# Optimization experiments

Hardware: AMD Instinct MI355X
Metric: run time of the kernel (lower is better)

## Reference

```python
import jax, jax.numpy as jnp
import numpy as np

N = 50000   # nodes
E = 800000  # edges
D = 64      # attrs_dim
H = 128     # 2*attrs_dim (GIN MLP hidden)
L = 3       # gnn_layers_num
G = 128     # graphs in batch


def setup_inputs() -> dict:
    key = jax.random.key(0)
    ks = jax.random.split(key, 9)
    s = 0.1
    attrs = jax.random.normal(ks[0], (N, D), dtype=jnp.float32)
    edge_index = jax.random.randint(ks[1], (2, E), 0, N, dtype=jnp.int64)
    batch = jnp.sort(jax.random.randint(ks[2], (N,), 0, G, dtype=jnp.int64))
    W1 = jax.random.normal(ks[3], (L, D, H), dtype=jnp.float32) * s
    b1 = jnp.zeros((L, H), jnp.float32)
    W2 = jax.random.normal(ks[4], (L, H, H), dtype=jnp.float32) * s
    b2 = jnp.zeros((L, H), jnp.float32)
    W3 = jax.random.normal(ks[5], (L, H, D), dtype=jnp.float32) * s
    b3 = jnp.zeros((L, D), jnp.float32)
    return {"attrs": attrs, "W1": W1, "b1": b1, "W2": W2, "b2": b2,
            "W3": W3, "b3": b3, "edge_index": edge_index, "batch": batch}


def reference(attrs, W1, b1, W2, b2, W3, b3, edge_index, batch):
    src, dst = edge_index[0], edge_index[1]
    x = attrs
    for l in range(L):  # small fixed layer count
        # GINConv with eps=0: MLP(x + sum_{j->i} x_j)
        agg = jax.ops.segment_sum(x[src], dst, num_segments=N)
        h = x + agg
        # MLP with tanh after each linear (per MLP.forward)
        h = jnp.tanh(h @ W1[l] + b1[l])
        h = jnp.tanh(h @ W2[l] + b2[l])
        h = jnp.tanh(h @ W3[l] + b3[l])
        # outer activation in GNN.forward
        x = jnp.tanh(h)
    # scatter_mean over graph ids
    sums = jax.ops.segment_sum(x, batch, num_segments=G)          # [G, D]
    counts = jax.ops.segment_sum(jnp.ones((N,), x.dtype), batch, num_segments=G)
    return sums / jnp.maximum(counts, 1.0)[:, None]
```

## Files before the change

kernel.cpp:

```cpp
#include <hip/hip_runtime.h>
#include <math.h>

#define N_NODES 50000
#define N_EDGES 800000
#define DIM 64
#define HID 128
#define LAYERS 3
#define NGRAPH 128

#define SCAN_TILE 1024
#define SCAN_NB ((N_NODES + SCAN_TILE - 1) / SCAN_TILE)

typedef __attribute__((ext_vector_type(8))) short short8v;
typedef __attribute__((ext_vector_type(4))) float f32x4;

__device__ __forceinline__ float bf2f(unsigned short u) {
    return __uint_as_float(((unsigned)u) << 16);
}
__device__ __forceinline__ unsigned short f2bf(float x) {
    unsigned u = __float_as_uint(x);
    unsigned r = (u + 0x7fff + ((u >> 16) & 1)) >> 16;
    return (unsigned short)r;
}
__device__ __forceinline__ float fast_tanh(float x) {
    float xc = fminf(fmaxf(x, -9.0f), 9.0f);
    float y = __expf(2.0f * xc);
    return 1.0f - 2.0f * __builtin_amdgcn_rcpf(y + 1.0f);
}

__global__ void count_kernel(const int* __restrict__ dst,
                             int* __restrict__ counts,
                             unsigned short* __restrict__ rank) {
    int e = (blockIdx.x * blockDim.x + threadIdx.x) * 2;
    if (e + 1 < N_EDGES) {
        int d0 = dst[e], d1 = dst[e + 1];
        int r0 = atomicAdd(&counts[d0], 1);
        int r1 = atomicAdd(&counts[d1], 1);
        rank[e]     = (unsigned short)r0;
        rank[e + 1] = (unsigned short)r1;
    } else if (e < N_EDGES) {
        rank[e] = (unsigned short)atomicAdd(&counts[dst[e]], 1);
    }
}

__global__ void scan_partial_kernel(const int* __restrict__ counts,
                                    int* __restrict__ bsum) {
    __shared__ int red[256];
    const int b = blockIdx.x, tid = threadIdx.x;
    const int base = b * SCAN_TILE + tid * 4;
    int s = 0;
    if (base + 3 < N_NODES) {
        int4 v = *reinterpret_cast<const int4*>(counts + base);
        s = v.x + v.y + v.z + v.w;
    } else {
        for (int i = 0; i < 4; ++i)
            if (base + i < N_NODES) s += counts[base + i];
    }
    red[tid] = s;
    __syncthreads();
    for (int off = 128; off > 0; off >>= 1) {
        if (tid < off) red[tid] += red[tid + off];
        __syncthreads();
    }
    if (tid == 0) bsum[b] = red[0];
}

__global__ void scan_mid_kernel(const int* __restrict__ bsum,
                                int* __restrict__ bpre,
                                int* __restrict__ offsets) {
    int tid = threadIdx.x;
    int orig = (tid < SCAN_NB) ? bsum[tid] : 0;
    int v = orig;
    for (int off = 1; off < 64; off <<= 1) {
        int u = __shfl_up(v, off);
        if (tid >= off) v += u;
    }
    if (tid < SCAN_NB) bpre[tid] = v - orig;
    if (tid == 0) offsets[N_NODES] = N_EDGES;
}

__global__ void scan_final_kernel(const int* __restrict__ counts,
                                  const int* __restrict__ bpre,
                                  int* __restrict__ offsets) {
    __shared__ int pre[256];
    const int b = blockIdx.x, tid = threadIdx.x;
    const int base = b * SCAN_TILE + tid * 4;
    int c[4];
    int s = 0;
#pragma unroll
    for (int i = 0; i < 4; ++i) {
        c[i] = (base + i < N_NODES) ? counts[base + i] : 0;
        s += c[i];
    }
    pre[tid] = s;
    __syncthreads();
    for (int off = 1; off < 256; off <<= 1) {
        int v = (tid >= off) ? pre[tid - off] : 0;
        __syncthreads();
        pre[tid] += v;
        __syncthreads();
    }
    int run = bpre[b] + pre[tid] - s;
#pragma unroll
    for (int i = 0; i < 4; ++i) {
        if (base + i < N_NODES) {
            offsets[base + i] = run;
            run += c[i];
        }
    }
}

__global__ void place_kernel(const int* __restrict__ src,
                             const int* __restrict__ dst,
                             const unsigned short* __restrict__ rank,
                             const int* __restrict__ offsets,
                             unsigned short* __restrict__ csr_src) {
    int e = blockIdx.x * blockDim.x + threadIdx.x;
    if (e >= N_EDGES) return;
    csr_src[offsets[dst[e]] + (int)rank[e]] = (unsigned short)src[e];
}

template<int K, int C>
__device__ __forceinline__ void repack_one(const float* __restrict__ W,
                                           unsigned short* __restrict__ P, int t) {
    constexpr int KT = K / 32, CT = C / 16;
    int lane = t & 63; int rest = t >> 6;
    int ct = rest % CT; rest /= CT;
    int kt = rest % KT; int l = rest / KT;
    int li = lane & 15, hi = lane >> 4;
    const float* Wl = W + (size_t)l * K * C;
    short8v o;
#pragma unroll
    for (int j = 0; j < 8; ++j)
        o[j] = (short)f2bf(Wl[(size_t)(kt * 32 + hi * 8 + j) * C + ct * 16 + li]);
    *reinterpret_cast<short8v*>(P + ((size_t)l * KT * CT * 64 + (size_t)(kt * CT + ct) * 64 + lane) * 8) = o;
}

__global__ void repack_all_kernel(const float* __restrict__ W1, const float* __restrict__ W2,
                                  const float* __restrict__ W3,
                                  unsigned short* __restrict__ P1, unsigned short* __restrict__ P2,
                                  unsigned short* __restrict__ P3) {
    int t = blockIdx.x * 256 + threadIdx.x;
    if (t < 3072)       repack_one<DIM, HID>(W1, P1, t);
    else if (t < 9216)  repack_one<HID, HID>(W2, P2, t - 3072);
    else                repack_one<HID, DIM>(W3, P3, t - 9216);
}

template<bool F32IN, bool LAST>
__global__ __launch_bounds__(256) void gnn_layer_kernel(
        const float* __restrict__ xf, const unsigned short* __restrict__ xb,
        const int* __restrict__ offsets, const unsigned short* __restrict__ csr_src,
        const unsigned short* __restrict__ pw1, const float* __restrict__ bias1,
        const unsigned short* __restrict__ pw2, const float* __restrict__ bias2,
        const unsigned short* __restrict__ pw3, const float* __restrict__ bias3,
        unsigned short* __restrict__ outx,
        const int* __restrict__ batch, float* __restrict__ psums) {
    __shared__ float aggA[16 * 68];
    __shared__ float aggB[16 * 68];
    __shared__ unsigned short tileA[16 * 128];
    __shared__ unsigned short tileB[16 * 128];
    __shared__ int soff[17];
    const int tid = threadIdx.x;
    const int wave = tid >> 6, lane = tid & 63;
    const int li = lane & 15, hi = lane >> 4;
    const int r0 = blockIdx.x * 16;
    char* tA = reinterpret_cast<char*>(tileA);
    char* tB = reinterpret_cast<char*>(tileB);

    if (tid < 17) soff[tid] = offsets[r0 + tid];
    __syncthreads();

    {
        const int g  = tid >> 3;
        const int nr = g >> 1;
        const int h  = g & 1;
        const int q  = tid & 7;
        const int n  = r0 + nr;
        float a[8];
        if (h == 0) {
            if (F32IN) {
                const float* xr = xf + (size_t)n * DIM + q * 8;
                float4 u = *reinterpret_cast<const float4*>(xr);
                float4 w = *reinterpret_cast<const float4*>(xr + 4);
                a[0]=u.x; a[1]=u.y; a[2]=u.z; a[3]=u.w;
                a[4]=w.x; a[5]=w.y; a[6]=w.z; a[7]=w.w;
            } else {
                short8v v = *reinterpret_cast<const short8v*>(xb + (size_t)n * DIM + q * 8);
#pragma unroll
                for (int j = 0; j < 8; ++j) a[j] = bf2f((unsigned short)v[j]);
            }
        } else {
#pragma unroll
            for (int j = 0; j < 8; ++j) a[j] = 0.f;
        }
        const int p0 = soff[nr], pe1 = soff[nr + 1];
        const int mid = p0 + ((pe1 - p0 + 1) >> 1);
        int p        = h ? mid : p0;
        const int pe = h ? pe1 : mid;
        for (; p + 4 <= pe; p += 4) {
            int s0 = csr_src[p + 0];
            int s1 = csr_src[p + 1];
            int s2 = csr_src[p + 2];
            int s3 = csr_src[p + 3];
            if (F32IN) {
                const float* x0 = xf + (size_t)s0 * DIM + q * 8;
                const float* x1 = xf + (size_t)s1 * DIM + q * 8;
                const float* x2 = xf + (size_t)s2 * DIM + q * 8;
                const float* x3 = xf + (size_t)s3 * DIM + q * 8;
                float4 u0 = *reinterpret_cast<const float4*>(x0);
                float4 w0 = *reinterpret_cast<const float4*>(x0 + 4);
                float4 u1 = *reinterpret_cast<const float4*>(x1);
                float4 w1 = *reinterpret_cast<const float4*>(x1 + 4);
                float4 u2 = *reinterpret_cast<const float4*>(x2);
                float4 w2 = *reinterpret_cast<const float4*>(x2 + 4);
                float4 u3 = *reinterpret_cast<const float4*>(x3);
                float4 w3 = *reinterpret_cast<const float4*>(x3 + 4);
                a[0] += u0.x + u1.x + u2.x + u3.x;
                a[1] += u0.y + u1.y + u2.y + u3.y;
                a[2] += u0.z + u1.z + u2.z + u3.z;
                a[3] += u0.w + u1.w + u2.w + u3.w;
                a[4] += w0.x + w1.x + w2.x + w3.x;
                a[5] += w0.y + w1.y + w2.y + w3.y;
                a[6] += w0.z + w1.z + w2.z + w3.z;
                a[7] += w0.w + w1.w + w2.w + w3.w;
            } else {
                short8v v0 = *reinterpret_cast<const short8v*>(xb + (size_t)s0 * DIM + q * 8);
                short8v v1 = *reinterpret_cast<const short8v*>(xb + (size_t)s1 * DIM + q * 8);
                short8v v2 = *reinterpret_cast<const short8v*>(xb + (size_t)s2 * DIM + q * 8);
                short8v v3 = *reinterpret_cast<const short8v*>(xb + (size_t)s3 * DIM + q * 8);
#pragma unroll
                for (int j = 0; j < 8; ++j)
                    a[j] += bf2f((unsigned short)v0[j]) + bf2f((unsigned short)v1[j])
                          + bf2f((unsigned short)v2[j]) + bf2f((unsigned short)v3[j]);
            }
        }
        for (; p < pe; ++p) {
            int s = csr_src[p];
            if (F32IN) {
                const float* xs = xf + (size_t)s * DIM + q * 8;
                float4 u = *reinterpret_cast<const float4*>(xs);
                float4 w = *reinterpret_cast<const float4*>(xs + 4);
                a[0] += u.x; a[1] += u.y; a[2] += u.z; a[3] += u.w;
                a[4] += w.x; a[5] += w.y; a[6] += w.z; a[7] += w.w;
            } else {
                short8v v = *reinterpret_cast<const short8v*>(xb + (size_t)s * DIM + q * 8);
#pragma unroll
                for (int j = 0; j < 8; ++j) a[j] += bf2f((unsigned short)v[j]);
            }
        }
        float* d = (h ? aggB : aggA) + nr * 68 + q * 8;
        *reinterpret_cast<f32x4*>(d)     = (f32x4){a[0], a[1], a[2], a[3]};
        *reinterpret_cast<f32x4*>(d + 4) = (f32x4){a[4], a[5], a[6], a[7]};
    }
    __syncthreads();

    short8v af[2];
#pragma unroll
    for (int kt = 0; kt < 2; ++kt) {
        const float* sA = &aggA[li * 68 + kt * 32 + hi * 8];
        const float* sB = &aggB[li * 68 + kt * 32 + hi * 8];
#pragma unroll
        for (int j = 0; j < 8; ++j) af[kt][j] = (short)f2bf(sA[j] + sB[j]);
    }

    f32x4 acc1[2];
#pragma unroll
    for (int c = 0; c < 2; ++c) acc1[c] = (f32x4){0.f, 0.f, 0.f, 0.f};
#pragma unroll
    for (int c = 0; c < 2; ++c) {
        const int ct = 2 * wave + c;
#pragma unroll
        for (int kt = 0; kt < 2; ++kt) {
            short8v bfr = *reinterpret_cast<const short8v*>(pw1 + ((size_t)(kt * 8 + ct) * 64 + lane) * 8);
            acc1[c] = __builtin_amdgcn_mfma_f32_16x16x32_bf16(af[kt], bfr, acc1[c], 0, 0, 0);
        }
    }
#pragma unroll
    for (int c = 0; c < 2; ++c) {
        const int ct = 2 * wave + c;
        float bv = bias1[ct * 16 + li];
#pragma unroll
        for (int j = 0; j < 4; ++j) {
            int row = hi * 4 + j;
            unsigned off = (unsigned)(row * 256 + (ct * 16 + li) * 2) ^ ((unsigned)(row & 7) << 4);
            *reinterpret_cast<unsigned short*>(tA + off) = f2bf(fast_tanh(acc1[c][j] + bv));
        }
    }
    __syncthreads();

    short8v af2[4];
#pragma unroll
    for (int kt = 0; kt < 4; ++kt) {
        unsigned off = (unsigned)(li * 256 + (kt * 32 + hi * 8) * 2) ^ ((unsigned)(li & 7) << 4);
        af2[kt] = *reinterpret_cast<const short8v*>(tA + off);
    }
    f32x4 acc2[2];
#pragma unroll
    for (int c = 0; c < 2; ++c) acc2[c] = (f32x4){0.f, 0.f, 0.f, 0.f};
#pragma unroll
    for (int c = 0; c < 2; ++c) {
        const int ct = 2 * wave + c;
#pragma unroll
        for (int kt = 0; kt < 4; ++kt) {
            short8v bfr = *reinterpret_cast<const short8v*>(pw2 + ((size_t)(kt * 8 + ct) * 64 + lane) * 8);
            acc2[c] = __builtin_amdgcn_mfma_f32_16x16x32_bf16(af2[kt], bfr, acc2[c], 0, 0, 0);
        }
    }
#pragma unroll
    for (int c = 0; c < 2; ++c) {
        const int ct = 2 * wave + c;
        float bv = bias2[ct * 16 + li];
#pragma unroll
        for (int j = 0; j < 4; ++j) {
            int row = hi * 4 + j;
            unsigned off = (unsigned)(row * 256 + (ct * 16 + li) * 2) ^ ((unsigned)(row & 7) << 4);
            *reinterpret_cast<unsigned short*>(tB + off) = f2bf(fast_tanh(acc2[c][j] + bv));
        }
    }
    __syncthreads();

    short8v af3[4];
#pragma unroll
    for (int kt = 0; kt < 4; ++kt) {
        unsigned off = (unsigned)(li * 256 + (kt * 32 + hi * 8) * 2) ^ ((unsigned)(li & 7) << 4);
        af3[kt] = *reinterpret_cast<const short8v*>(tB + off);
    }
    f32x4 acc3 = (f32x4){0.f, 0.f, 0.f, 0.f};
#pragma unroll
    for (int kt = 0; kt < 4; ++kt) {
        short8v bfr = *reinterpret_cast<const short8v*>(pw3 + ((size_t)(kt * 4 + wave) * 64 + lane) * 8);
        acc3 = __builtin_amdgcn_mfma_f32_16x16x32_bf16(af3[kt], bfr, acc3, 0, 0, 0);
    }
    {
        const int c = wave * 16 + li;
        float bv = bias3[c];
        if (LAST) {
            const int row0 = r0 + hi * 4;
            float v[4];
#pragma unroll
            for (int j = 0; j < 4; ++j) v[j] = fast_tanh(fast_tanh(acc3[j] + bv));
            int g = batch[row0];
            float acc = v[0];
#pragma unroll
            for (int j = 1; j < 4; ++j) {
                int gj = batch[row0 + j];
                if (gj == g) acc += v[j];
                else {
                    atomicAdd(&psums[g * DIM + c], acc);
                    g = gj; acc = v[j];
                }
            }
            atomicAdd(&psums[g * DIM + c], acc);
        } else {
#pragma unroll
            for (int j = 0; j < 4; ++j) {
                int row = r0 + hi * 4 + j;
                float vv = fast_tanh(fast_tanh(acc3[j] + bv));
                outx[(size_t)row * DIM + c] = f2bf(vv);
            }
        }
    }
}

__global__ void pool_final_kernel(const float* __restrict__ sums,
                                  const int* __restrict__ batch,
                                  float* __restrict__ out) {
    const int g = blockIdx.x;
    const int d = threadIdx.x;
    int lo = 0, hi = N_NODES;
    while (lo < hi) { int m = (lo + hi) >> 1; if (batch[m] < g) lo = m + 1; else hi = m; }
    int start = lo;
    hi = N_NODES;
    while (lo < hi) { int m = (lo + hi) >> 1; if (batch[m] < g + 1) lo = m + 1; else hi = m; }
    float cnt = (float)(lo - start);
    out[g * DIM + d] = sums[g * DIM + d] / fmaxf(cnt, 1.f);
}

extern "C" void kernel_launch(void* const* d_in, const int* in_sizes, int n_in,
                              void* d_out, int out_size, void* d_ws, size_t ws_size,
                              hipStream_t stream) {
    const float* attrs = (const float*)d_in[0];
    const float* W1    = (const float*)d_in[1];
    const float* b1    = (const float*)d_in[2];
    const float* W2    = (const float*)d_in[3];
    const float* b2    = (const float*)d_in[4];
    const float* W3    = (const float*)d_in[5];
    const float* b3    = (const float*)d_in[6];
    const int* edge_index = (const int*)d_in[7];
    const int* batch      = (const int*)d_in[8];
    float* out = (float*)d_out;

    unsigned short* buf0 = (unsigned short*)d_ws;
    unsigned short* buf1 = buf0 + (size_t)N_NODES * DIM;
    unsigned short* pW1  = buf1 + (size_t)N_NODES * DIM;
    unsigned short* pW2  = pW1 + 24576;
    unsigned short* pW3  = pW2 + 49152;
    float* psums  = (float*)(pW3 + 24576);
    int* offsets  = (int*)(psums + NGRAPH * DIM);
    unsigned short* csr16 = (unsigned short*)(offsets + N_NODES + 1);
    unsigned short* rank  = csr16 + N_EDGES;
    int* counts   = (int*)(rank + N_EDGES);
    int* bsum     = counts + N_NODES;
    int* bpre     = bsum + SCAN_NB;

    const int* src = edge_index;
    const int* dst = edge_index + N_EDGES;

    const int edge_blocks  = (N_EDGES + 255) / 256;
    const int count_blocks = (N_EDGES / 2 + 255) / 256;
    const int gnn_blocks   = N_NODES / 16;

    hipMemsetAsync(counts, 0, (size_t)N_NODES * sizeof(int), stream);
    hipMemsetAsync(psums, 0, (size_t)NGRAPH * DIM * sizeof(float), stream);
    count_kernel<<<count_blocks, 256, 0, stream>>>(dst, counts, rank);
    scan_partial_kernel<<<SCAN_NB, 256, 0, stream>>>(counts, bsum);
    scan_mid_kernel<<<1, 64, 0, stream>>>(bsum, bpre, offsets);
    scan_final_kernel<<<SCAN_NB, 256, 0, stream>>>(counts, bpre, offsets);
    place_kernel<<<edge_blocks, 256, 0, stream>>>(src, dst, rank, offsets, csr16);

    repack_all_kernel<<<48, 256, 0, stream>>>(W1, W2, W3, pW1, pW2, pW3);

    for (int l = 0; l < LAYERS; ++l) {
        const unsigned short* w1 = pW1 + (size_t)l * 2 * 8 * 64 * 8;
        const unsigned short* w2 = pW2 + (size_t)l * 4 * 8 * 64 * 8;
        const unsigned short* w3 = pW3 + (size_t)l * 4 * 4 * 64 * 8;
        const float* bb1 = b1 + (size_t)l * HID;
        const float* bb2 = b2 + (size_t)l * HID;
        const float* bb3 = b3 + (size_t)l * DIM;
        if (l == 0)
            gnn_layer_kernel<true, false><<<gnn_blocks, 256, 0, stream>>>(
                attrs, nullptr, offsets, csr16, w1, bb1, w2, bb2, w3, bb3,
                buf0, nullptr, nullptr);
        else if (l == 1)
            gnn_layer_kernel<false, false><<<gnn_blocks, 256, 0, stream>>>(
                nullptr, buf0, offsets, csr16, w1, bb1, w2, bb2, w3, bb3,
                buf1, nullptr, nullptr);
        else
            gnn_layer_kernel<false, true><<<gnn_blocks, 256, 0, stream>>>(
                nullptr, buf1, offsets, csr16, w1, bb1, w2, bb2, w3, bb3,
                nullptr, batch, psums);
    }

    pool_final_kernel<<<NGRAPH, DIM, 0, stream>>>(psums, batch, out);
}
```

Before: 183.4 us.

## Convert input to bf16, split aggregation 4-way with 512-thread blocks, fuse scan

Adds a pre-pass that converts the fp32 node attributes to bf16, so the first layer gathers half as many bytes per neighbour. The GNN layer kernel now runs 512 threads per 16-node tile, splits each node's edge list into four quarters instead of two, and gives each of 8 waves one MFMA column tile. The separate scan_mid kernel is removed: each scan_final block sums the preceding block totals serially. place_kernel now handles two edges per thread. The costs are an extra conversion kernel, bf16 rounding of the layer-0 input, and idle waves during the third matmul.

New measurement: 195.9 us. 6.8% more time.

```diff
diff --git a/kernel.cpp b/kernel.cpp
--- a/kernel.cpp
+++ b/kernel.cpp
@@ -26,6 +26,19 @@
     float xc = fminf(fmaxf(x, -9.0f), 9.0f);
     float y = __expf(2.0f * xc);
     return 1.0f - 2.0f * __builtin_amdgcn_rcpf(y + 1.0f);
+}
+
+__global__ void cvt_kernel(const float* __restrict__ a, unsigned short* __restrict__ b) {
+    int i = blockIdx.x * blockDim.x + threadIdx.x;
+    if (i >= N_NODES * DIM / 8) return;
+    const float4* p = reinterpret_cast<const float4*>(a + (size_t)i * 8);
+    float4 u = p[0], w = p[1];
+    short8v o;
+    o[0] = (short)f2bf(u.x); o[1] = (short)f2bf(u.y);
+    o[2] = (short)f2bf(u.z); o[3] = (short)f2bf(u.w);
+    o[4] = (short)f2bf(w.x); o[5] = (short)f2bf(w.y);
+    o[6] = (short)f2bf(w.z); o[7] = (short)f2bf(w.w);
+    *reinterpret_cast<short8v*>(b + (size_t)i * 8) = o;
 }
 
 __global__ void count_kernel(const int* __restrict__ dst,
@@ -65,25 +78,18 @@
     if (tid == 0) bsum[b] = red[0];
 }
 
-__global__ void scan_mid_kernel(const int* __restrict__ bsum,
-                                int* __restrict__ bpre,
-                                int* __restrict__ offsets) {
-    int tid = threadIdx.x;
-    int orig = (tid < SCAN_NB) ? bsum[tid] : 0;
-    int v = orig;
-    for (int off = 1; off < 64; off <<= 1) {
-        int u = __shfl_up(v, off);
-        if (tid >= off) v += u;
-    }
-    if (tid < SCAN_NB) bpre[tid] = v - orig;
-    if (tid == 0) offsets[N_NODES] = N_EDGES;
-}
-
 __global__ void scan_final_kernel(const int* __restrict__ counts,
-                                  const int* __restrict__ bpre,
+                                  const int* __restrict__ bsum,
                                   int* __restrict__ offsets) {
     __shared__ int pre[256];
+    __shared__ int bbase;
     const int b = blockIdx.x, tid = threadIdx.x;
+    if (tid == 0) {
+        int s = 0;
+        for (int i = 0; i < b; ++i) s += bsum[i];
+        bbase = s;
+        if (b == SCAN_NB - 1) offsets[N_NODES] = N_EDGES;
+    }
     const int base = b * SCAN_TILE + tid * 4;
     int c[4];
     int s = 0;
@@ -100,7 +106,7 @@
         pre[tid] += v;
         __syncthreads();
     }
-    int run = bpre[b] + pre[tid] - s;
+    int run = bbase + pre[tid] - s;
 #pragma unroll
     for (int i = 0; i < 4; ++i) {
         if (base + i < N_NODES) {
@@ -115,9 +121,15 @@
                              const unsigned short* __restrict__ rank,
                              const int* __restrict__ offsets,
                              unsigned short* __restrict__ csr_src) {
-    int e = blockIdx.x * blockDim.x + threadIdx.x;
-    if (e >= N_EDGES) return;
-    csr_src[offsets[dst[e]] + (int)rank[e]] = (unsigned short)src[e];
+    int e = (blockIdx.x * blockDim.x + threadIdx.x) * 2;
+    if (e + 1 < N_EDGES) {
+        int d0 = dst[e], d1 = dst[e + 1];
+        int o0 = offsets[d0], o1 = offsets[d1];
+        csr_src[o0 + (int)rank[e]]     = (unsigned short)src[e];
+        csr_src[o1 + (int)rank[e + 1]] = (unsigned short)src[e + 1];
+    } else if (e < N_EDGES) {
+        csr_src[offsets[dst[e]] + (int)rank[e]] = (unsigned short)src[e];
+    }
 }
 
 template<int K, int C>
@@ -146,17 +158,16 @@
     else                repack_one<HID, DIM>(W3, P3, t - 9216);
 }
 
-template<bool F32IN, bool LAST>
-__global__ __launch_bounds__(256) void gnn_layer_kernel(
-        const float* __restrict__ xf, const unsigned short* __restrict__ xb,
+template<bool LAST>
+__global__ __launch_bounds__(512) void gnn_layer_kernel(
+        const unsigned short* __restrict__ xb,
         const int* __restrict__ offsets, const unsigned short* __restrict__ csr_src,
         const unsigned short* __restrict__ pw1, const float* __restrict__ bias1,
         const unsigned short* __restrict__ pw2, const float* __restrict__ bias2,
         const unsigned short* __restrict__ pw3, const float* __restrict__ bias3,
         unsigned short* __restrict__ outx,
         const int* __restrict__ batch, float* __restrict__ psums) {
-    __shared__ float aggA[16 * 68];
-    __shared__ float aggB[16 * 68];
+    __shared__ float aggQ[4][16 * 68];
     __shared__ unsigned short tileA[16 * 128];
     __shared__ unsigned short tileB[16 * 128];
     __shared__ int soff[17];
@@ -172,118 +183,75 @@
 
     {
         const int g  = tid >> 3;
-        const int nr = g >> 1;
-        const int h  = g & 1;
+        const int nr = g >> 2;
+        const int h  = g & 3;
         const int q  = tid & 7;
         const int n  = r0 + nr;
         float a[8];
         if (h == 0) {
-            if (F32IN) {
-                const float* xr = xf + (size_t)n * DIM + q * 8;
-                float4 u = *reinterpret_cast<const float4*>(xr);
-                float4 w = *reinterpret_cast<const float4*>(xr + 4);
-                a[0]=u.x; a[1]=u.y; a[2]=u.z; a[3]=u.w;
-                a[4]=w.x; a[5]=w.y; a[6]=w.z; a[7]=w.w;
-            } else {
-                short8v v = *reinterpret_cast<const short8v*>(xb + (size_t)n * DIM + q * 8);
-#pragma unroll
-                for (int j = 0; j < 8; ++j) a[j] = bf2f((unsigned short)v[j]);
-            }
+            short8v v = *reinterpret_cast<const short8v*>(xb + (size_t)n * DIM + q * 8);
+#pragma unroll
+            for (int j = 0; j < 8; ++j) a[j] = bf2f((unsigned short)v[j]);
         } else {
 #pragma unroll
             for (int j = 0; j < 8; ++j) a[j] = 0.f;
         }
-        const int p0 = soff[nr], pe1 = soff[nr + 1];
-        const int mid = p0 + ((pe1 - p0 + 1) >> 1);
-        int p        = h ? mid : p0;
-        const int pe = h ? pe1 : mid;
+        const int p0 = soff[nr];
+        const int d  = soff[nr + 1] - p0;
+        int p        = p0 + ((d * h) >> 2);
+        const int pe = p0 + ((d * (h + 1)) >> 2);
         for (; p + 4 <= pe; p += 4) {
             int s0 = csr_src[p + 0];
             int s1 = csr_src[p + 1];
             int s2 = csr_src[p + 2];
             int s3 = csr_src[p + 3];
-            if (F32IN) {
-                const float* x0 = xf + (size_t)s0 * DIM + q * 8;
-                const float* x1 = xf + (size_t)s1 * DIM + q * 8;
-                const float* x2 = xf + (size_t)s2 * DIM + q * 8;
-                const float* x3 = xf + (size_t)s3 * DIM + q * 8;
-                float4 u0 = *reinterpret_cast<const float4*>(x0);
-                float4 w0 = *reinterpret_cast<const float4*>(x0 + 4);
-                float4 u1 = *reinterpret_cast<const float4*>(x1);
-                float4 w1 = *reinterpret_cast<const float4*>(x1 + 4);
-                float4 u2 = *reinterpret_cast<const float4*>(x2);
-                float4 w2 = *reinterpret_cast<const float4*>(x2 + 4);
-                float4 u3 = *reinterpret_cast<const float4*>(x3);
-                float4 w3 = *reinterpret_cast<const float4*>(x3 + 4);
-                a[0] += u0.x + u1.x + u2.x + u3.x;
-                a[1] += u0.y + u1.y + u2.y + u3.y;
-                a[2] += u0.z + u1.z + u2.z + u3.z;
-                a[3] += u0.w + u1.w + u2.w + u3.w;
-                a[4] += w0.x + w1.x + w2.x + w3.x;
-                a[5] += w0.y + w1.y + w2.y + w3.y;
-                a[6] += w0.z + w1.z + w2.z + w3.z;
-                a[7] += w0.w + w1.w + w2.w + w3.w;
-            } else {
-                short8v v0 = *reinterpret_cast<const short8v*>(xb + (size_t)s0 * DIM + q * 8);
-                short8v v1 = *reinterpret_cast<const short8v*>(xb + (size_t)s1 * DIM + q * 8);
-                short8v v2 = *reinterpret_cast<const short8v*>(xb + (size_t)s2 * DIM + q * 8);
-                short8v v3 = *reinterpret_cast<const short8v*>(xb + (size_t)s3 * DIM + q * 8);
-#pragma unroll
-                for (int j = 0; j < 8; ++j)
-                    a[j] += bf2f((unsigned short)v0[j]) + bf2f((unsigned short)v1[j])
-                          + bf2f((unsigned short)v2[j]) + bf2f((unsigned short)v3[j]);
-            }
+            short8v v0 = *reinterpret_cast<const short8v*>(xb + (size_t)s0 * DIM + q * 8);
+            short8v v1 = *reinterpret_cast<const short8v*>(xb + (size_t)s1 * DIM + q * 8);
+            short8v v2 = *reinterpret_cast<const short8v*>(xb + (size_t)s2 * DIM + q * 8);
+            short8v v3 = *reinterpret_cast<const short8v*>(xb + (size_t)s3 * DIM + q * 8);
+#pragma unroll
+            for (int j = 0; j < 8; ++j)
+                a[j] += bf2f((unsigned short)v0[j]) + bf2f((unsigned short)v1[j])
+                      + bf2f((unsigned short)v2[j]) + bf2f((unsigned short)v3[j]);
         }
         for (; p < pe; ++p) {
             int s = csr_src[p];
-            if (F32IN) {
-                const float* xs = xf + (size_t)s * DIM + q * 8;
-                float4 u = *reinterpret_cast<const float4*>(xs);
-                float4 w = *reinterpret_cast<const float4*>(xs + 4);
-                a[0] += u.x; a[1] += u.y; a[2] += u.z; a[3] += u.w;
-                a[4] += w.x; a[5] += w.y; a[6] += w.z; a[7] += w.w;
-            } else {
-                short8v v = *reinterpret_cast<const short8v*>(xb + (size_t)s * DIM + q * 8);
-#pragma unroll
-                for (int j = 0; j < 8; ++j) a[j] += bf2f((unsigned short)v[j]);
-            }
-        }
-        float* d = (h ? aggB : aggA) + nr * 68 + q * 8;
-        *reinterpret_cast<f32x4*>(d)     = (f32x4){a[0], a[1], a[2], a[3]};
-        *reinterpret_cast<f32x4*>(d + 4) = (f32x4){a[4], a[5], a[6], a[7]};
+            short8v v = *reinterpret_cast<const short8v*>(xb + (size_t)s * DIM + q * 8);
+#pragma unroll
+            for (int j = 0; j < 8; ++j) a[j] += bf2f((unsigned short)v[j]);
+        }
+        float* dq = &aggQ[h][nr * 68 + q * 8];
+        *reinterpret_cast<f32x4*>(dq)     = (f32x4){a[0], a[1], a[2], a[3]};
+        *reinterpret_cast<f32x4*>(dq + 4) = (f32x4){a[4], a[5], a[6], a[7]};
     }
     __syncthreads();
 
     short8v af[2];
 #pragma unroll
     for (int kt = 0; kt < 2; ++kt) {
-        const float* sA = &aggA[li * 68 + kt * 32 + hi * 8];
-        const float* sB = &aggB[li * 68 + kt * 32 + hi * 8];
-#pragma unroll
-        for (int j = 0; j < 8; ++j) af[kt][j] = (short)f2bf(sA[j] + sB[j]);
-    }
-
-    f32x4 acc1[2];
-#pragma unroll
-    for (int c = 0; c < 2; ++c) acc1[c] = (f32x4){0.f, 0.f, 0.f, 0.f};
-#pragma unroll
-    for (int c = 0; c < 2; ++c) {
-        const int ct = 2 * wave + c;
+        const float* s0 = &aggQ[0][li * 68 + kt * 32 + hi * 8];
+        const float* s1 = &aggQ[1][li * 68 + kt * 32 + hi * 8];
+        const float* s2 = &aggQ[2][li * 68 + kt * 32 + hi * 8];
+        const float* s3 = &aggQ[3][li * 68 + kt * 32 + hi * 8];
+#pragma unroll
+        for (int j = 0; j < 8; ++j)
+            af[kt][j] = (short)f2bf((s0[j] + s1[j]) + (s2[j] + s3[j]));
+    }
+
+    {
+        const int ct = wave;
+        f32x4 acc1 = (f32x4){0.f, 0.f, 0.f, 0.f};
 #pragma unroll
         for (int kt = 0; kt < 2; ++kt) {
             short8v bfr = *reinterpret_cast<const short8v*>(pw1 + ((size_t)(kt * 8 + ct) * 64 + lane) * 8);
-            acc1[c] = __builtin_amdgcn_mfma_f32_16x16x32_bf16(af[kt], bfr, acc1[c], 0, 0, 0);
-        }
-    }
-#pragma unroll
-    for (int c = 0; c < 2; ++c) {
-        const int ct = 2 * wave + c;
+            acc1 = __builtin_amdgcn_mfma_f32_16x16x32_bf16(af[kt], bfr, acc1, 0, 0, 0);
+        }
         float bv = bias1[ct * 16 + li];
 #pragma unroll
         for (int j = 0; j < 4; ++j) {
             int row = hi * 4 + j;
             unsigned off = (unsigned)(row * 256 + (ct * 16 + li) * 2) ^ ((unsigned)(row & 7) << 4);
-            *reinterpret_cast<unsigned short*>(tA + off) = f2bf(fast_tanh(acc1[c][j] + bv));
+            *reinterpret_cast<unsigned short*>(tA + off) = f2bf(fast_tanh(acc1[j] + bv));
         }
     }
     __syncthreads();
@@ -294,44 +262,37 @@
         unsigned off = (unsigned)(li * 256 + (kt * 32 + hi * 8) * 2) ^ ((unsigned)(li & 7) << 4);
         af2[kt] = *reinterpret_cast<const short8v*>(tA + off);
     }
-    f32x4 acc2[2];
-#pragma unroll
-    for (int c = 0; c < 2; ++c) acc2[c] = (f32x4){0.f, 0.f, 0.f, 0.f};
-#pragma unroll
-    for (int c = 0; c < 2; ++c) {
-        const int ct = 2 * wave + c;
+    {
+        const int ct = wave;
+        f32x4 acc2 = (f32x4){0.f, 0.f, 0.f, 0.f};
 #pragma unroll
         for (int kt = 0; kt < 4; ++kt) {
             short8v bfr = *reinterpret_cast<const short8v*>(pw2 + ((size_t)(kt * 8 + ct) * 64 + lane) * 8);
-            acc2[c] = __builtin_amdgcn_mfma_f32_16x16x32_bf16(af2[kt], bfr, acc2[c], 0, 0, 0);
-        }
-    }
-#pragma unroll
-    for (int c = 0; c < 2; ++c) {
-        const int ct = 2 * wave + c;
+            acc2 = __builtin_amdgcn_mfma_f32_16x16x32_bf16(af2[kt], bfr, acc2, 0, 0, 0);
+        }
         float bv = bias2[ct * 16 + li];
 #pragma unroll
         for (int j = 0; j < 4; ++j) {
             int row = hi * 4 + j;
             unsigned off = (unsigned)(row * 256 + (ct * 16 + li) * 2) ^ ((unsigned)(row & 7) << 4);
-            *reinterpret_cast<unsigned short*>(tB + off) = f2bf(fast_tanh(acc2[c][j] + bv));
-        }
-    }
-    __syncthreads();
-
-    short8v af3[4];
-#pragma unroll
-    for (int kt = 0; kt < 4; ++kt) {
-        unsigned off = (unsigned)(li * 256 + (kt * 32 + hi * 8) * 2) ^ ((unsigned)(li & 7) << 4);
-        af3[kt] = *reinterpret_cast<const short8v*>(tB + off);
-    }
-    f32x4 acc3 = (f32x4){0.f, 0.f, 0.f, 0.f};
-#pragma unroll
-    for (int kt = 0; kt < 4; ++kt) {
-        short8v bfr = *reinterpret_cast<const short8v*>(pw3 + ((size_t)(kt * 4 + wave) * 64 + lane) * 8);
-        acc3 = __builtin_amdgcn_mfma_f32_16x16x32_bf16(af3[kt], bfr, acc3, 0, 0, 0);
-    }
-    {
+            *reinterpret_cast<unsigned short*>(tB + off) = f2bf(fast_tanh(acc2[j] + bv));
+        }
+    }
+    __syncthreads();
+
+    if (wave < 4) {
+        short8v af3[4];
+#pragma unroll
+        for (int kt = 0; kt < 4; ++kt) {
+            unsigned off = (unsigned)(li * 256 + (kt * 32 + hi * 8) * 2) ^ ((unsigned)(li & 7) << 4);
+            af3[kt] = *reinterpret_cast<const short8v*>(tB + off);
+        }
+        f32x4 acc3 = (f32x4){0.f, 0.f, 0.f, 0.f};
+#pragma unroll
+        for (int kt = 0; kt < 4; ++kt) {
+            short8v bfr = *reinterpret_cast<const short8v*>(pw3 + ((size_t)(kt * 4 + wave) * 64 + lane) * 8);
+            acc3 = __builtin_amdgcn_mfma_f32_16x16x32_bf16(af3[kt], bfr, acc3, 0, 0, 0);
+        }
         const int c = wave * 16 + li;
         float bv = bias3[c];
         if (LAST) {
@@ -390,9 +351,10 @@
     const int* batch      = (const int*)d_in[8];
     float* out = (float*)d_out;
 
-    unsigned short* buf0 = (unsigned short*)d_ws;
-    unsigned short* buf1 = buf0 + (size_t)N_NODES * DIM;
-    unsigned short* pW1  = buf1 + (size_t)N_NODES * DIM;
+    unsigned short* buf0   = (unsigned short*)d_ws;
+    unsigned short* buf1   = buf0 + (size_t)N_NODES * DIM;
+    unsigned short* attrsb = buf1 + (size_t)N_NODES * DIM;
+    unsigned short* pW1  = attrsb + (size_t)N_NODES * DIM;
     unsigned short* pW2  = pW1 + 24576;
     unsigned short* pW3  = pW2 + 49152;
     float* psums  = (float*)(pW3 + 24576);
@@ -401,23 +363,21 @@
     unsigned short* rank  = csr16 + N_EDGES;
     int* counts   = (int*)(rank + N_EDGES);
     int* bsum     = counts + N_NODES;
-    int* bpre     = bsum + SCAN_NB;
 
     const int* src = edge_index;
     const int* dst = edge_index + N_EDGES;
 
-    const int edge_blocks  = (N_EDGES + 255) / 256;
-    const int count_blocks = (N_EDGES / 2 + 255) / 256;
-    const int gnn_blocks   = N_NODES / 16;
+    const int pair_blocks = (N_EDGES / 2 + 255) / 256;
+    const int gnn_blocks  = N_NODES / 16;
+    const int cvt_blocks  = (N_NODES * DIM / 8 + 255) / 256;
 
     hipMemsetAsync(counts, 0, (size_t)N_NODES * sizeof(int), stream);
     hipMemsetAsync(psums, 0, (size_t)NGRAPH * DIM * sizeof(float), stream);
-    count_kernel<<<count_blocks, 256, 0, stream>>>(dst, counts, rank);
+    cvt_kernel<<<cvt_blocks, 256, 0, stream>>>(attrs, attrsb);
+    count_kernel<<<pair_blocks, 256, 0, stream>>>(dst, counts, rank);
     scan_partial_kernel<<<SCAN_NB, 256, 0, stream>>>(counts, bsum);
-    scan_mid_kernel<<<1, 64, 0, stream>>>(bsum, bpre, offsets);
-    scan_final_kernel<<<SCAN_NB, 256, 0, stream>>>(counts, bpre, offsets);
-    place_kernel<<<edge_blocks, 256, 0, stream>>>(src, dst, rank, offsets, csr16);
-
+    scan_final_kernel<<<SCAN_NB, 256, 0, stream>>>(counts, bsum, offsets);
+    place_kernel<<<pair_blocks, 256, 0, stream>>>(src, dst, rank, offsets, csr16);
     repack_all_kernel<<<48, 256, 0, stream>>>(W1, W2, W3, pW1, pW2, pW3);
 
     for (int l = 0; l < LAYERS; ++l) {
@@ -428,16 +388,16 @@
         const float* bb2 = b2 + (size_t)l * HID;
         const float* bb3 = b3 + (size_t)l * DIM;
         if (l == 0)
-            gnn_layer_kernel<true, false><<<gnn_blocks, 256, 0, stream>>>(
-                attrs, nullptr, offsets, csr16, w1, bb1, w2, bb2, w3, bb3,
+            gnn_layer_kernel<false><<<gnn_blocks, 512, 0, stream>>>(
+                attrsb, offsets, csr16, w1, bb1, w2, bb2, w3, bb3,
                 buf0, nullptr, nullptr);
         else if (l == 1)
-            gnn_layer_kernel<false, false><<<gnn_blocks, 256, 0, stream>>>(
-                nullptr, buf0, offsets, csr16, w1, bb1, w2, bb2, w3, bb3,
+            gnn_layer_kernel<false><<<gnn_blocks, 512, 0, stream>>>(
+                buf0, offsets, csr16, w1, bb1, w2, bb2, w3, bb3,
                 buf1, nullptr, nullptr);
         else
-            gnn_layer_kernel<false, true><<<gnn_blocks, 256, 0, stream>>>(
-                nullptr, buf1, offsets, csr16, w1, bb1, w2, bb2, w3, bb3,
+            gnn_layer_kernel<true><<<gnn_blocks, 512, 0, stream>>>(
+                buf1, offsets, csr16, w1, bb1, w2, bb2, w3, bb3,
                 nullptr, batch, psums);
     }
 
```
